# Kernel tuning notes

Measured on AMD Instinct MI355X. Metric: run time of the kernel, lower is better.

The kernel has to match this reference:

```python
import jax, jax.numpy as jnp
import numpy as np

B, C, K, F = 16, 64, 128, 6
HORIZON_S = 3.0  # conflict_horizon_s default
EPS = 1e-06


def setup_inputs() -> dict:
    rng = np.random.default_rng(0)
    # base adjacency: sparse random directed graph, zero diagonal
    A = (rng.random((B, K, K)) < 0.05).astype(np.float32)
    A[:, np.arange(K), np.arange(K)] = 0.0
    # candidates: exactly one unordered-pair edit (state in {0:none,1:i->j,2:j->i})
    cand = np.repeat(A[:, None], C, axis=1).copy()
    i = rng.integers(0, K - 1, (B, C))
    j = i + 1 + (rng.integers(0, K - 1, (B, C)) % (K - 1 - i))
    state = rng.integers(0, 3, (B, C))
    bidx = np.arange(B)[:, None] * np.ones((1, C), dtype=np.int64)
    cidx = np.ones((B, 1), dtype=np.int64) * np.arange(C)[None, :]
    cand[bidx, cidx, i, j] = (state == 1).astype(np.float32)
    cand[bidx, cidx, j, i] = (state == 2).astype(np.float32)
    cand[:, 0] = A  # candidate 0 is NOOP (keep A_t)
    # agent features: (x, y, yaw, vx, vy, pad)
    feat = rng.normal(size=(B, K, F)).astype(np.float32)
    feat[..., 0:2] *= 20.0  # spread positions over ~40m
    mask = (rng.random((B, K)) > 0.1).astype(np.float32)
    return {
        "A_t": jnp.asarray(A),
        "candidate_A": jnp.asarray(cand),
        "agent_feat": jnp.asarray(feat),
        "agent_mask": jnp.asarray(mask),
    }


def _edit_tokens(A_t, candidate_A):
    # vectorized version of EBSTM.extract_edit_tokens
    Bn, Cn, Kn, _ = candidate_A.shape
    base = A_t > 0.5                      # [B,K,K]
    cb = candidate_A > 0.5                # [B,C,K,K]
    diff = cb != base[:, None]            # [B,C,K,K]
    upper = jnp.triu(jnp.ones((Kn, Kn), dtype=bool), k=1)
    pairdiff = (diff | jnp.swapaxes(diff, -1, -2)) & upper
    flat = pairdiff.reshape(Bn, Cn, Kn * Kn)
    changed = flat.any(-1)                # [B,C]
    idx = jnp.argmax(flat, axis=-1)       # first changed pair in row-major (i,j) order
    i = idx // Kn
    j = idx % Kn
    barange = jnp.arange(Bn)[:, None]
    carange = jnp.arange(Cn)[None, :]
    b_ij = base[barange, i, j]
    b_ji = base[barange, j, i]
    c_ij = cb[barange, carange, i, j]
    c_ji = cb[barange, carange, j, i]
    prev = jnp.where(b_ij & ~b_ji, 1, jnp.where(b_ji & ~b_ij, 2, 0))
    nxt = jnp.where(c_ij & ~c_ji, 1, jnp.where(c_ji & ~c_ij, 2, 0))
    tokens = jnp.stack([i, j, prev, nxt], axis=-1).astype(jnp.int32)
    return tokens * changed[..., None].astype(jnp.int32)


def _relation_state3(cb):
    # cb: bool [B,C,K,K]
    at = jnp.swapaxes(cb, -1, -2)
    return ((cb & ~at).astype(jnp.int32) * 1
            + (~cb & at).astype(jnp.int32) * 2
            + (cb & at).astype(jnp.int32) * 3)


def _batched_acyclic(cb, agent_mask):
    # vectorized Kahn zero-indegree peel, matching EBSTM._is_acyclic semantics:
    #  - indegree counts edges from ALL sources (valid or not)
    #  - only valid nodes are ever removed
    #  - special case: <=1 valid node is acyclic
    Bn, Cn, Kn, _ = cb.shape
    valid = (agent_mask > 0.5)[:, None, :]           # [B,1,K]
    Ai = cb.astype(jnp.int32)                        # [B,C,K,K]
    indeg = Ai.sum(axis=-2) * valid.astype(jnp.int32)  # [B,C,K]
    removed = jnp.zeros((Bn, Cn, Kn), dtype=bool)

    def body(t, carry):
        indeg, removed = carry
        rem = valid & (~removed) & (indeg == 0)
        dec = jnp.einsum('bci,bcij->bcj', rem.astype(jnp.int32), Ai)
        return indeg - dec, removed | rem

    indeg, removed = jax.lax.fori_loop(0, Kn, body, (indeg, removed))
    vcount = valid.astype(jnp.int32).sum(-1)          # [B,1]
    return (removed.astype(jnp.int32).sum(-1) == vcount) | (vcount <= 1)


def _pair_dists(agent_feat):
    pos = agent_feat[..., 0:2]
    vel = agent_feat[..., 3:5]
    # _pair_distance: d[b,i,j] = |pos_i - pos_j|
    d = jnp.linalg.norm(pos[:, :, None] - pos[:, None, :], axis=-1)
    # _pair_closest_approach_distance: r[b,i,j] = pos_j - pos_i
    r = pos[:, None, :] - pos[:, :, None]
    v = vel[:, None, :] - vel[:, :, None]
    vv = (v * v).sum(-1)
    rv = (r * v).sum(-1)
    t_star = jnp.clip(-rv / (vv + EPS), 0.0, HORIZON_S)
    dmin = jnp.linalg.norm(r + v * t_star[..., None], axis=-1)
    eye = jnp.eye(dmin.shape[-1], dtype=bool)[None]
    dmin = jnp.where(eye, jnp.inf, dmin)
    return jnp.stack([d, dmin], axis=0)  # [2,B,K,K]


def reference(A_t, candidate_A, agent_feat, agent_mask):
    cb = candidate_A > 0.5
    tokens = _edit_tokens(A_t, candidate_A)          # [B,C,4] int32
    rel = _relation_state3(cb)                       # [B,C,K,K] int32
    acyclic = _batched_acyclic(cb, agent_mask)       # [B,C] bool
    dists = _pair_dists(agent_feat)                  # [2,B,K,K] float32
    return tokens, rel, acyclic, dists
```

## Files before the change

### kernel.cpp

```cpp
#include <hip/hip_runtime.h>
#include <cstdint>
#include <math.h>

#define KN 128
#define BATCH 16
#define CAND 64

typedef float vfloat4 __attribute__((ext_vector_type(4)));

static constexpr size_t TOK_OFF = 0;
static constexpr size_t REL_OFF = (size_t)BATCH * CAND * 4;
static constexpr size_t ACY_OFF = REL_OFF + (size_t)BATCH * CAND * KN * KN;
static constexpr size_t DST_OFF = ACY_OFF + (size_t)BATCH * CAND;

#define DIAG_BIG 1.0e30f

__global__ __launch_bounds__(256) void fused_kernel(const float* __restrict__ A_t,
                                                    const float* __restrict__ cand,
                                                    const float* __restrict__ feat,
                                                    const float* __restrict__ mask,
                                                    float* __restrict__ out) {
    __shared__ uint32_t adj[KN][5];
    __shared__ uint32_t adjW[4][KN];
    __shared__ uint32_t baseB[KN][4];
    __shared__ int      indegP[2][KN];
    __shared__ int      indeg[KN];
    __shared__ uint32_t validW[4];
    __shared__ uint32_t remW[4];
    __shared__ uint32_t removedW[4];
    __shared__ int      minIdx;

    const int t    = threadIdx.x;
    const int lane = t & 63;
    const int wave = t >> 6;
    const int bc   = blockIdx.x;
    const int b    = bc >> 6;

    const float* cptr = cand + (size_t)bc * (KN * KN);
    const float* aptr = A_t + (size_t)b * (KN * KN);

    if (t == 0) minIdx = 0x7fffffff;
    if (t < 4)  removedW[t] = 0;

    if (wave < 2) {
        float mv = mask[b * KN + wave * 64 + lane];
        unsigned long long m = __ballot(mv > 0.5f);
        if (lane == 0) {
            validW[wave * 2]     = (uint32_t)m;
            validW[wave * 2 + 1] = (uint32_t)(m >> 32);
        }
    }

    for (int m = 0; m < 16; ++m) {
        int rowPair = m * 4 + wave;
        int r   = rowPair * 2 + (lane >> 5);
        int sub = lane & 31;
        const float4 v = ((const float4*)(aptr + (size_t)r * KN))[sub];
        uint32_t nib = (v.x > 0.5f ? 1u : 0u) | (v.y > 0.5f ? 2u : 0u) |
                       (v.z > 0.5f ? 4u : 0u) | (v.w > 0.5f ? 8u : 0u);
        uint32_t word = nib << (4 * (sub & 7));
        word |= __shfl_xor(word, 1);
        word |= __shfl_xor(word, 2);
        word |= __shfl_xor(word, 4);
        if ((lane & 7) == 0) baseB[r][sub >> 3] = word;
    }

    for (int m = 0; m < 16; ++m) {
        int rowPair = m * 4 + wave;
        int r   = rowPair * 2 + (lane >> 5);
        int sub = lane & 31;
        const float4 v = ((const float4*)(cptr + (size_t)r * KN))[sub];
        uint32_t nib = (v.x > 0.5f ? 1u : 0u) | (v.y > 0.5f ? 2u : 0u) |
                       (v.z > 0.5f ? 4u : 0u) | (v.w > 0.5f ? 8u : 0u);
        uint32_t word = nib << (4 * (sub & 7));
        word |= __shfl_xor(word, 1);
        word |= __shfl_xor(word, 2);
        word |= __shfl_xor(word, 4);
        if ((lane & 7) == 0) adj[r][sub >> 3] = word;
    }

    {
        int bi = 2 * bc + (t >> 7);
        int b2 = bi >> 7, i = bi & 127, j = t & 127;
        const float* fi = feat + (size_t)bi * 6;
        const float* fj = feat + (size_t)(b2 * KN + j) * 6;
        float pix = fi[0], piy = fi[1], vix = fi[3], viy = fi[4];
        float pjx = fj[0], pjy = fj[1], vjx = fj[3], vjy = fj[4];
        float dx = pix - pjx, dy = piy - pjy;
        float d = sqrtf(dx * dx + dy * dy);
        float rx = pjx - pix, ry = pjy - piy;
        float vx = vjx - vix, vy = vjy - viy;
        float vv = vx * vx + vy * vy;
        float rv = rx * vx + ry * vy;
        float ts = fminf(fmaxf(-rv / (vv + 1e-6f), 0.0f), 3.0f);
        float mx = rx + vx * ts, my = ry + vy * ts;
        float dmin = (i == j) ? DIAG_BIG : sqrtf(mx * mx + my * my);
        float* o = out + DST_OFF;
        __builtin_nontemporal_store(d,    o + (size_t)(b2 * KN + i) * KN + j);
        __builtin_nontemporal_store(dmin, o + (size_t)((BATCH + b2) * KN + i) * KN + j);
    }
    __syncthreads();

    for (int w = t; w < 512; w += 256) {
        int iw = w >> 7, j = w & 127;
        adjW[iw][j] = adj[j][iw];
    }

    {
        int j = t & 127, half = t >> 7;
        uint32_t jw = j >> 5, jb = j & 31;
        int s = 0;
        int i0 = half * 64;
        for (int i = i0; i < i0 + 64; ++i) s += (adj[i][jw] >> jb) & 1u;
        indegP[half][j] = s;
    }

    for (int idx = t; idx < 512; idx += 256) {
        int i = idx >> 2, k = idx & 3;
        uint32_t diff = adj[i][k] ^ baseB[i][k];
        if (diff) {
            int base = k * 32;
            uint32_t up, low;
            if (i < base)            { up = diff; low = 0u; }
            else if (i >= base + 31) { up = 0u; low = (i > base + 31) ? diff : (diff & 0x7fffffffu); }
            else {
                int s = i - base;
                up  = diff & (0xffffffffu << (s + 1));
                low = diff & ((1u << s) - 1u);
            }
            int c1 = 0x7fffffff, c2 = 0x7fffffff;
            if (up)  c1 = (i << 7) | (base + __builtin_ctz(up));
            if (low) { int cc = base + __builtin_ctz(low); c2 = (cc << 7) | i; }
            int cm = min(c1, c2);
            if (cm != 0x7fffffff) atomicMin(&minIdx, cm);
        }
    }
    __syncthreads();

    if (t < KN) {
        uint32_t jw = t >> 5, jb = t & 31;
        bool valid = (validW[jw] >> jb) & 1u;
        indeg[t] = valid ? (indegP[0][t] + indegP[1][t]) : 0;
    }

    if (t == 0) {
        float* tok = out + TOK_OFF + (size_t)bc * 4;
        int mi = minIdx;
        if (mi != 0x7fffffff) {
            int i = mi >> 7, j = mi & 127;
            uint32_t b_ij = (baseB[i][j >> 5] >> (j & 31)) & 1u;
            uint32_t b_ji = (baseB[j][i >> 5] >> (i & 31)) & 1u;
            uint32_t c_ij = (adj[i][j >> 5] >> (j & 31)) & 1u;
            uint32_t c_ji = (adj[j][i >> 5] >> (i & 31)) & 1u;
            int prev = (b_ij && !b_ji) ? 1 : ((b_ji && !b_ij) ? 2 : 0);
            int nxt  = (c_ij && !c_ji) ? 1 : ((c_ji && !c_ij) ? 2 : 0);
            tok[0] = (float)i; tok[1] = (float)j; tok[2] = (float)prev; tok[3] = (float)nxt;
        } else {
            tok[0] = 0.f; tok[1] = 0.f; tok[2] = 0.f; tok[3] = 0.f;
        }
    }

    {
        float* relp = out + REL_OFF + (size_t)bc * (KN * KN);
        for (int m = 0; m < 16; ++m) {
            int q  = t + 256 * m;
            int i  = q >> 5;
            int j0 = (q & 31) * 4;
            uint32_t wij = adj[i][j0 >> 5];
            int sh = j0 & 31;
            uint32_t iw = i >> 5, ib = i & 31;
            const uint4 wt = *(const uint4*)&adjW[iw][j0];
            vfloat4 o;
            o.x = (float)(((wij >> (sh + 0)) & 1u) + 2u * ((wt.x >> ib) & 1u));
            o.y = (float)(((wij >> (sh + 1)) & 1u) + 2u * ((wt.y >> ib) & 1u));
            o.z = (float)(((wij >> (sh + 2)) & 1u) + 2u * ((wt.z >> ib) & 1u));
            o.w = (float)(((wij >> (sh + 3)) & 1u) + 2u * ((wt.w >> ib) & 1u));
            __builtin_nontemporal_store(o, ((vfloat4*)relp) + q);
        }
    }
    __syncthreads();

    for (int it = 0; it < KN; ++it) {
        bool rem = false;
        if (t < KN) {
            uint32_t jw = t >> 5, jb = t & 31;
            bool valid   = (validW[jw] >> jb) & 1u;
            bool removed = (removedW[jw] >> jb) & 1u;
            rem = valid && !removed && (indeg[t] == 0);
        }
        unsigned long long m = __ballot(rem);
        if (wave < 2 && lane == 0) {
            remW[wave * 2]     = (uint32_t)m;
            remW[wave * 2 + 1] = (uint32_t)(m >> 32);
        }
        __syncthreads();
        uint32_t r0 = remW[0], r1 = remW[1], r2 = remW[2], r3 = remW[3];
        if ((r0 | r1 | r2 | r3) == 0u) break;
        if (t < 4) removedW[t] |= remW[t];
        if (t < KN) {
            uint32_t jw = t >> 5, jb = t & 31;
            int dec = 0;
            uint32_t rw[4] = {r0, r1, r2, r3};
            for (int w = 0; w < 4; ++w) {
                uint32_t mm = rw[w];
                while (mm) {
                    int i = w * 32 + __builtin_ctz(mm);
                    mm &= mm - 1;
                    dec += (adj[i][jw] >> jb) & 1u;
                }
            }
            indeg[t] -= dec;
        }
        __syncthreads();
    }
    __syncthreads();

    if (t == 0) {
        int rc = __popc(removedW[0]) + __popc(removedW[1]) + __popc(removedW[2]) + __popc(removedW[3]);
        int vc = __popc(validW[0]) + __popc(validW[1]) + __popc(validW[2]) + __popc(validW[3]);
        out[ACY_OFF + bc] = ((rc == vc) || (vc <= 1)) ? 1.0f : 0.0f;
    }
}

extern "C" void kernel_launch(void* const* d_in, const int* in_sizes, int n_in,
                              void* d_out, int out_size, void* d_ws, size_t ws_size,
                              hipStream_t stream) {
    const float* A_t  = (const float*)d_in[0];
    const float* cand = (const float*)d_in[1];
    const float* feat = (const float*)d_in[2];
    const float* mask = (const float*)d_in[3];
    float* out = (float*)d_out;

    fused_kernel<<<BATCH * CAND, 256, 0, stream>>>(A_t, cand, feat, mask, out);
}
```

Baseline: 137.1 us.

## Precompute base adjacency bitmasks in a pre-kernel and prefetch candidate rows into registers

Measured after the change: 121.1 us. 11.6% less time.

```diff
diff --git a/kernel.cpp b/kernel.cpp
--- a/kernel.cpp
+++ b/kernel.cpp
@@ -15,11 +15,26 @@
 
 #define DIAG_BIG 1.0e30f
 
-__global__ __launch_bounds__(256) void fused_kernel(const float* __restrict__ A_t,
-                                                    const float* __restrict__ cand,
-                                                    const float* __restrict__ feat,
-                                                    const float* __restrict__ mask,
-                                                    float* __restrict__ out) {
+__global__ __launch_bounds__(256) void base_bits_kernel(const float* __restrict__ A_t,
+                                                        uint32_t* __restrict__ bits) {
+    int tid  = blockIdx.x * 256 + threadIdx.x;
+    int wave = tid >> 6;
+    int lane = tid & 63;
+    int half = wave & 1;
+    int row  = wave >> 1;
+    float v = A_t[(size_t)row * KN + half * 64 + lane];
+    unsigned long long m = __ballot(v > 0.5f);
+    if (lane == 0) {
+        bits[row * 4 + half * 2]     = (uint32_t)m;
+        bits[row * 4 + half * 2 + 1] = (uint32_t)(m >> 32);
+    }
+}
+
+__global__ __launch_bounds__(256) void main_kernel(const float* __restrict__ cand,
+                                                   const float* __restrict__ feat,
+                                                   const float* __restrict__ mask,
+                                                   const uint32_t* __restrict__ baseBits,
+                                                   float* __restrict__ out) {
     __shared__ uint32_t adj[KN][5];
     __shared__ uint32_t adjW[4][KN];
     __shared__ uint32_t baseB[KN][4];
@@ -37,10 +52,21 @@
     const int b    = bc >> 6;
 
     const float* cptr = cand + (size_t)bc * (KN * KN);
-    const float* aptr = A_t + (size_t)b * (KN * KN);
+
+    float4 c[16];
+    const int sub = lane & 31;
+    #pragma unroll
+    for (int m = 0; m < 16; ++m) {
+        int r = (m * 4 + wave) * 2 + (lane >> 5);
+        c[m] = ((const float4*)(cptr + (size_t)r * KN))[sub];
+    }
 
     if (t == 0) minIdx = 0x7fffffff;
     if (t < 4)  removedW[t] = 0;
+
+    for (int w = t; w < 512; w += 256) {
+        baseB[w >> 2][w & 3] = baseBits[b * 512 + w];
+    }
 
     if (wave < 2) {
         float mv = mask[b * KN + wave * 64 + lane];
@@ -49,34 +75,6 @@
             validW[wave * 2]     = (uint32_t)m;
             validW[wave * 2 + 1] = (uint32_t)(m >> 32);
         }
-    }
-
-    for (int m = 0; m < 16; ++m) {
-        int rowPair = m * 4 + wave;
-        int r   = rowPair * 2 + (lane >> 5);
-        int sub = lane & 31;
-        const float4 v = ((const float4*)(aptr + (size_t)r * KN))[sub];
-        uint32_t nib = (v.x > 0.5f ? 1u : 0u) | (v.y > 0.5f ? 2u : 0u) |
-                       (v.z > 0.5f ? 4u : 0u) | (v.w > 0.5f ? 8u : 0u);
-        uint32_t word = nib << (4 * (sub & 7));
-        word |= __shfl_xor(word, 1);
-        word |= __shfl_xor(word, 2);
-        word |= __shfl_xor(word, 4);
-        if ((lane & 7) == 0) baseB[r][sub >> 3] = word;
-    }
-
-    for (int m = 0; m < 16; ++m) {
-        int rowPair = m * 4 + wave;
-        int r   = rowPair * 2 + (lane >> 5);
-        int sub = lane & 31;
-        const float4 v = ((const float4*)(cptr + (size_t)r * KN))[sub];
-        uint32_t nib = (v.x > 0.5f ? 1u : 0u) | (v.y > 0.5f ? 2u : 0u) |
-                       (v.z > 0.5f ? 4u : 0u) | (v.w > 0.5f ? 8u : 0u);
-        uint32_t word = nib << (4 * (sub & 7));
-        word |= __shfl_xor(word, 1);
-        word |= __shfl_xor(word, 2);
-        word |= __shfl_xor(word, 4);
-        if ((lane & 7) == 0) adj[r][sub >> 3] = word;
     }
 
     {
@@ -99,6 +97,19 @@
         __builtin_nontemporal_store(d,    o + (size_t)(b2 * KN + i) * KN + j);
         __builtin_nontemporal_store(dmin, o + (size_t)((BATCH + b2) * KN + i) * KN + j);
     }
+
+    #pragma unroll
+    for (int m = 0; m < 16; ++m) {
+        int r = (m * 4 + wave) * 2 + (lane >> 5);
+        const float4 v = c[m];
+        uint32_t nib = (v.x > 0.5f ? 1u : 0u) | (v.y > 0.5f ? 2u : 0u) |
+                       (v.z > 0.5f ? 4u : 0u) | (v.w > 0.5f ? 8u : 0u);
+        uint32_t word = nib << (4 * (sub & 7));
+        word |= __shfl_xor(word, 1);
+        word |= __shfl_xor(word, 2);
+        word |= __shfl_xor(word, 4);
+        if ((lane & 7) == 0) adj[r][sub >> 3] = word;
+    }
     __syncthreads();
 
     for (int w = t; w < 512; w += 256) {
@@ -162,6 +173,7 @@
 
     {
         float* relp = out + REL_OFF + (size_t)bc * (KN * KN);
+        #pragma unroll 4
         for (int m = 0; m < 16; ++m) {
             int q  = t + 256 * m;
             int i  = q >> 5;
@@ -230,6 +242,8 @@
     const float* feat = (const float*)d_in[2];
     const float* mask = (const float*)d_in[3];
     float* out = (float*)d_out;
-
-    fused_kernel<<<BATCH * CAND, 256, 0, stream>>>(A_t, cand, feat, mask, out);
+    uint32_t* bits = (uint32_t*)d_ws;
+
+    base_bits_kernel<<<1024, 256, 0, stream>>>(A_t, bits);
+    main_kernel<<<BATCH * CAND, 256, 0, stream>>>(cand, feat, mask, bits, out);
 }
```

## Split fused kernel into specialized block roles for rel, acyclic, and distances

Applied to the files above, without the earlier changes.

After: 136.3 us. Within noise of the previous version (-0.6%).

```diff
diff --git a/kernel.cpp b/kernel.cpp
--- a/kernel.cpp
+++ b/kernel.cpp
@@ -15,13 +15,12 @@
 
 #define DIAG_BIG 1.0e30f
 
-__global__ __launch_bounds__(256) void fused_kernel(const float* __restrict__ A_t,
-                                                    const float* __restrict__ cand,
-                                                    const float* __restrict__ feat,
-                                                    const float* __restrict__ mask,
-                                                    float* __restrict__ out) {
+__global__ __launch_bounds__(256) void mega_kernel(const float* __restrict__ A_t,
+                                                   const float* __restrict__ cand,
+                                                   const float* __restrict__ feat,
+                                                   const float* __restrict__ mask,
+                                                   float* __restrict__ out) {
     __shared__ uint32_t adj[KN][5];
-    __shared__ uint32_t adjW[4][KN];
     __shared__ uint32_t baseB[KN][4];
     __shared__ int      indegP[2][KN];
     __shared__ int      indeg[KN];
@@ -29,58 +28,230 @@
     __shared__ uint32_t remW[4];
     __shared__ uint32_t removedW[4];
     __shared__ int      minIdx;
+    __shared__ uint32_t adjH[64][5];
+    __shared__ uint32_t adjTW[2][KN];
 
     const int t    = threadIdx.x;
     const int lane = t & 63;
     const int wave = t >> 6;
-    const int bc   = blockIdx.x;
-    const int b    = bc >> 6;
-
-    const float* cptr = cand + (size_t)bc * (KN * KN);
-    const float* aptr = A_t + (size_t)b * (KN * KN);
-
-    if (t == 0) minIdx = 0x7fffffff;
-    if (t < 4)  removedW[t] = 0;
-
-    if (wave < 2) {
-        float mv = mask[b * KN + wave * 64 + lane];
-        unsigned long long m = __ballot(mv > 0.5f);
-        if (lane == 0) {
-            validW[wave * 2]     = (uint32_t)m;
-            validW[wave * 2 + 1] = (uint32_t)(m >> 32);
-        }
-    }
-
-    for (int m = 0; m < 16; ++m) {
-        int rowPair = m * 4 + wave;
-        int r   = rowPair * 2 + (lane >> 5);
-        int sub = lane & 31;
-        const float4 v = ((const float4*)(aptr + (size_t)r * KN))[sub];
-        uint32_t nib = (v.x > 0.5f ? 1u : 0u) | (v.y > 0.5f ? 2u : 0u) |
-                       (v.z > 0.5f ? 4u : 0u) | (v.w > 0.5f ? 8u : 0u);
-        uint32_t word = nib << (4 * (sub & 7));
-        word |= __shfl_xor(word, 1);
-        word |= __shfl_xor(word, 2);
-        word |= __shfl_xor(word, 4);
-        if ((lane & 7) == 0) baseB[r][sub >> 3] = word;
-    }
-
-    for (int m = 0; m < 16; ++m) {
-        int rowPair = m * 4 + wave;
-        int r   = rowPair * 2 + (lane >> 5);
-        int sub = lane & 31;
-        const float4 v = ((const float4*)(cptr + (size_t)r * KN))[sub];
-        uint32_t nib = (v.x > 0.5f ? 1u : 0u) | (v.y > 0.5f ? 2u : 0u) |
-                       (v.z > 0.5f ? 4u : 0u) | (v.w > 0.5f ? 8u : 0u);
-        uint32_t word = nib << (4 * (sub & 7));
-        word |= __shfl_xor(word, 1);
-        word |= __shfl_xor(word, 2);
-        word |= __shfl_xor(word, 4);
-        if ((lane & 7) == 0) adj[r][sub >> 3] = word;
-    }
-
-    {
-        int bi = 2 * bc + (t >> 7);
+    const int blk  = blockIdx.x;
+
+    if (blk < 2048) {
+        const int bc = blk >> 1;
+        const int h  = blk & 1;
+        const float* cptr = cand + (size_t)bc * (KN * KN);
+
+        float4 cr[8], cc[8];
+        const int sub   = lane & 31;
+        const int sub16 = lane & 15;
+        #pragma unroll
+        for (int m = 0; m < 8; ++m) {
+            int r = (m * 4 + wave) * 2 + (lane >> 5);
+            cr[m] = ((const float4*)(cptr + (size_t)(h * 64 + r) * KN))[sub];
+        }
+        #pragma unroll
+        for (int m = 0; m < 8; ++m) {
+            int j = m * 16 + wave * 4 + (lane >> 4);
+            cc[m] = ((const float4*)(cptr + (size_t)j * KN + h * 64))[sub16];
+        }
+
+        #pragma unroll
+        for (int m = 0; m < 8; ++m) {
+            int r = (m * 4 + wave) * 2 + (lane >> 5);
+            float4 v = cr[m];
+            uint32_t nib = (v.x > 0.5f ? 1u : 0u) | (v.y > 0.5f ? 2u : 0u) |
+                           (v.z > 0.5f ? 4u : 0u) | (v.w > 0.5f ? 8u : 0u);
+            uint32_t word = nib << (4 * (sub & 7));
+            word |= __shfl_xor(word, 1);
+            word |= __shfl_xor(word, 2);
+            word |= __shfl_xor(word, 4);
+            if ((lane & 7) == 0) adjH[r][sub >> 3] = word;
+        }
+        #pragma unroll
+        for (int m = 0; m < 8; ++m) {
+            int j = m * 16 + wave * 4 + (lane >> 4);
+            float4 v = cc[m];
+            uint32_t nib = (v.x > 0.5f ? 1u : 0u) | (v.y > 0.5f ? 2u : 0u) |
+                           (v.z > 0.5f ? 4u : 0u) | (v.w > 0.5f ? 8u : 0u);
+            uint32_t word = nib << (4 * (sub16 & 7));
+            word |= __shfl_xor(word, 1);
+            word |= __shfl_xor(word, 2);
+            word |= __shfl_xor(word, 4);
+            if ((sub16 & 7) == 0) adjTW[sub16 >> 3][j] = word;
+        }
+        __syncthreads();
+
+        float* relp = out + REL_OFF + (size_t)bc * (KN * KN);
+        #pragma unroll
+        for (int m = 0; m < 8; ++m) {
+            int q  = t + 256 * m;
+            int il = q >> 5;
+            int j0 = (q & 31) * 4;
+            uint32_t wij = adjH[il][j0 >> 5];
+            int sh = j0 & 31;
+            uint32_t ib = il & 31;
+            const uint4 wt = *(const uint4*)&adjTW[il >> 5][j0];
+            vfloat4 o;
+            o.x = (float)(((wij >> (sh + 0)) & 1u) + 2u * ((wt.x >> ib) & 1u));
+            o.y = (float)(((wij >> (sh + 1)) & 1u) + 2u * ((wt.y >> ib) & 1u));
+            o.z = (float)(((wij >> (sh + 2)) & 1u) + 2u * ((wt.z >> ib) & 1u));
+            o.w = (float)(((wij >> (sh + 3)) & 1u) + 2u * ((wt.w >> ib) & 1u));
+            __builtin_nontemporal_store(o, ((vfloat4*)relp) + (size_t)h * 2048 + q);
+        }
+    } else if (blk < 3072) {
+        const int bc = blk - 2048;
+        const int b  = bc >> 6;
+        const float* cptr = cand + (size_t)bc * (KN * KN);
+        const float* aptr = A_t + (size_t)b * (KN * KN);
+        const int sub = lane & 31;
+
+        float4 c[16];
+        #pragma unroll
+        for (int m = 0; m < 16; ++m) {
+            int r = (m * 4 + wave) * 2 + (lane >> 5);
+            c[m] = ((const float4*)(cptr + (size_t)r * KN))[sub];
+        }
+
+        if (t == 0) minIdx = 0x7fffffff;
+        if (t < 4)  removedW[t] = 0;
+
+        if (wave < 2) {
+            float mv = mask[b * KN + wave * 64 + lane];
+            unsigned long long m = __ballot(mv > 0.5f);
+            if (lane == 0) {
+                validW[wave * 2]     = (uint32_t)m;
+                validW[wave * 2 + 1] = (uint32_t)(m >> 32);
+            }
+        }
+
+        #pragma unroll
+        for (int m = 0; m < 16; ++m) {
+            int r = (m * 4 + wave) * 2 + (lane >> 5);
+            float4 v = c[m];
+            uint32_t nib = (v.x > 0.5f ? 1u : 0u) | (v.y > 0.5f ? 2u : 0u) |
+                           (v.z > 0.5f ? 4u : 0u) | (v.w > 0.5f ? 8u : 0u);
+            uint32_t word = nib << (4 * (sub & 7));
+            word |= __shfl_xor(word, 1);
+            word |= __shfl_xor(word, 2);
+            word |= __shfl_xor(word, 4);
+            if ((lane & 7) == 0) adj[r][sub >> 3] = word;
+        }
+        #pragma unroll
+        for (int m = 0; m < 16; ++m) {
+            int r = (m * 4 + wave) * 2 + (lane >> 5);
+            c[m] = ((const float4*)(aptr + (size_t)r * KN))[sub];
+        }
+        #pragma unroll
+        for (int m = 0; m < 16; ++m) {
+            int r = (m * 4 + wave) * 2 + (lane >> 5);
+            float4 v = c[m];
+            uint32_t nib = (v.x > 0.5f ? 1u : 0u) | (v.y > 0.5f ? 2u : 0u) |
+                           (v.z > 0.5f ? 4u : 0u) | (v.w > 0.5f ? 8u : 0u);
+            uint32_t word = nib << (4 * (sub & 7));
+            word |= __shfl_xor(word, 1);
+            word |= __shfl_xor(word, 2);
+            word |= __shfl_xor(word, 4);
+            if ((lane & 7) == 0) baseB[r][sub >> 3] = word;
+        }
+        __syncthreads();
+
+        {
+            int j = t & 127, half = t >> 7;
+            uint32_t jw = j >> 5, jb = j & 31;
+            int s = 0;
+            int i0 = half * 64;
+            for (int i = i0; i < i0 + 64; ++i) s += (adj[i][jw] >> jb) & 1u;
+            indegP[half][j] = s;
+        }
+
+        for (int idx = t; idx < 512; idx += 256) {
+            int i = idx >> 2, k = idx & 3;
+            uint32_t diff = adj[i][k] ^ baseB[i][k];
+            if (diff) {
+                int base = k * 32;
+                uint32_t up, low;
+                if (i < base)            { up = diff; low = 0u; }
+                else if (i >= base + 31) { up = 0u; low = (i > base + 31) ? diff : (diff & 0x7fffffffu); }
+                else {
+                    int s = i - base;
+                    up  = diff & (0xffffffffu << (s + 1));
+                    low = diff & ((1u << s) - 1u);
+                }
+                int c1 = 0x7fffffff, c2 = 0x7fffffff;
+                if (up)  c1 = (i << 7) | (base + __builtin_ctz(up));
+                if (low) { int cc = base + __builtin_ctz(low); c2 = (cc << 7) | i; }
+                int cm = min(c1, c2);
+                if (cm != 0x7fffffff) atomicMin(&minIdx, cm);
+            }
+        }
+        __syncthreads();
+
+        if (t < KN) {
+            uint32_t jw = t >> 5, jb = t & 31;
+            bool valid = (validW[jw] >> jb) & 1u;
+            indeg[t] = valid ? (indegP[0][t] + indegP[1][t]) : 0;
+        }
+
+        if (t == 0) {
+            float* tok = out + TOK_OFF + (size_t)bc * 4;
+            int mi = minIdx;
+            if (mi != 0x7fffffff) {
+                int i = mi >> 7, j = mi & 127;
+                uint32_t b_ij = (baseB[i][j >> 5] >> (j & 31)) & 1u;
+                uint32_t b_ji = (baseB[j][i >> 5] >> (i & 31)) & 1u;
+                uint32_t c_ij = (adj[i][j >> 5] >> (j & 31)) & 1u;
+                uint32_t c_ji = (adj[j][i >> 5] >> (i & 31)) & 1u;
+                int prev = (b_ij && !b_ji) ? 1 : ((b_ji && !b_ij) ? 2 : 0);
+                int nxt  = (c_ij && !c_ji) ? 1 : ((c_ji && !c_ij) ? 2 : 0);
+                tok[0] = (float)i; tok[1] = (float)j; tok[2] = (float)prev; tok[3] = (float)nxt;
+            } else {
+                tok[0] = 0.f; tok[1] = 0.f; tok[2] = 0.f; tok[3] = 0.f;
+            }
+        }
+        __syncthreads();
+
+        for (int it = 0; it < KN; ++it) {
+            bool rem = false;
+            if (t < KN) {
+                uint32_t jw = t >> 5, jb = t & 31;
+                bool valid   = (validW[jw] >> jb) & 1u;
+                bool removed = (removedW[jw] >> jb) & 1u;
+                rem = valid && !removed && (indeg[t] == 0);
+            }
+            unsigned long long m = __ballot(rem);
+            if (wave < 2 && lane == 0) {
+                remW[wave * 2]     = (uint32_t)m;
+                remW[wave * 2 + 1] = (uint32_t)(m >> 32);
+            }
+            __syncthreads();
+            uint32_t r0 = remW[0], r1 = remW[1], r2 = remW[2], r3 = remW[3];
+            if ((r0 | r1 | r2 | r3) == 0u) break;
+            if (t < 4) removedW[t] |= remW[t];
+            if (t < KN) {
+                uint32_t jw = t >> 5, jb = t & 31;
+                int dec = 0;
+                uint32_t rw[4] = {r0, r1, r2, r3};
+                for (int w = 0; w < 4; ++w) {
+                    uint32_t mm = rw[w];
+                    while (mm) {
+                        int i = w * 32 + __builtin_ctz(mm);
+                        mm &= mm - 1;
+                        dec += (adj[i][jw] >> jb) & 1u;
+                    }
+                }
+                indeg[t] -= dec;
+            }
+            __syncthreads();
+        }
+        __syncthreads();
+
+        if (t == 0) {
+            int rc = __popc(removedW[0]) + __popc(removedW[1]) + __popc(removedW[2]) + __popc(removedW[3]);
+            int vc = __popc(validW[0]) + __popc(validW[1]) + __popc(validW[2]) + __popc(validW[3]);
+            out[ACY_OFF + bc] = ((rc == vc) || (vc <= 1)) ? 1.0f : 0.0f;
+        }
+    } else {
+        int bi = 2 * (blk - 3072) + (t >> 7);
         int b2 = bi >> 7, i = bi & 127, j = t & 127;
         const float* fi = feat + (size_t)bi * 6;
         const float* fj = feat + (size_t)(b2 * KN + j) * 6;
@@ -99,127 +270,6 @@
         __builtin_nontemporal_store(d,    o + (size_t)(b2 * KN + i) * KN + j);
         __builtin_nontemporal_store(dmin, o + (size_t)((BATCH + b2) * KN + i) * KN + j);
     }
-    __syncthreads();
-
-    for (int w = t; w < 512; w += 256) {
-        int iw = w >> 7, j = w & 127;
-        adjW[iw][j] = adj[j][iw];
-    }
-
-    {
-        int j = t & 127, half = t >> 7;
-        uint32_t jw = j >> 5, jb = j & 31;
-        int s = 0;
-        int i0 = half * 64;
-        for (int i = i0; i < i0 + 64; ++i) s += (adj[i][jw] >> jb) & 1u;
-        indegP[half][j] = s;
-    }
-
-    for (int idx = t; idx < 512; idx += 256) {
-        int i = idx >> 2, k = idx & 3;
-        uint32_t diff = adj[i][k] ^ baseB[i][k];
-        if (diff) {
-            int base = k * 32;
-            uint32_t up, low;
-            if (i < base)            { up = diff; low = 0u; }
-            else if (i >= base + 31) { up = 0u; low = (i > base + 31) ? diff : (diff & 0x7fffffffu); }
-            else {
-                int s = i - base;
-                up  = diff & (0xffffffffu << (s + 1));
-                low = diff & ((1u << s) - 1u);
-            }
-            int c1 = 0x7fffffff, c2 = 0x7fffffff;
-            if (up)  c1 = (i << 7) | (base + __builtin_ctz(up));
-            if (low) { int cc = base + __builtin_ctz(low); c2 = (cc << 7) | i; }
-            int cm = min(c1, c2);
-            if (cm != 0x7fffffff) atomicMin(&minIdx, cm);
-        }
-    }
-    __syncthreads();
-
-    if (t < KN) {
-        uint32_t jw = t >> 5, jb = t & 31;
-        bool valid = (validW[jw] >> jb) & 1u;
-        indeg[t] = valid ? (indegP[0][t] + indegP[1][t]) : 0;
-    }
-
-    if (t == 0) {
-        float* tok = out + TOK_OFF + (size_t)bc * 4;
-        int mi = minIdx;
-        if (mi != 0x7fffffff) {
-            int i = mi >> 7, j = mi & 127;
-            uint32_t b_ij = (baseB[i][j >> 5] >> (j & 31)) & 1u;
-            uint32_t b_ji = (baseB[j][i >> 5] >> (i & 31)) & 1u;
-            uint32_t c_ij = (adj[i][j >> 5] >> (j & 31)) & 1u;
-            uint32_t c_ji = (adj[j][i >> 5] >> (i & 31)) & 1u;
-            int prev = (b_ij && !b_ji) ? 1 : ((b_ji && !b_ij) ? 2 : 0);
-            int nxt  = (c_ij && !c_ji) ? 1 : ((c_ji && !c_ij) ? 2 : 0);
-            tok[0] = (float)i; tok[1] = (float)j; tok[2] = (float)prev; tok[3] = (float)nxt;
-        } else {
-            tok[0] = 0.f; tok[1] = 0.f; tok[2] = 0.f; tok[3] = 0.f;
-        }
-    }
-
-    {
-        float* relp = out + REL_OFF + (size_t)bc * (KN * KN);
-        for (int m = 0; m < 16; ++m) {
-            int q  = t + 256 * m;
-            int i  = q >> 5;
-            int j0 = (q & 31) * 4;
-            uint32_t wij = adj[i][j0 >> 5];
-            int sh = j0 & 31;
-            uint32_t iw = i >> 5, ib = i & 31;
-            const uint4 wt = *(const uint4*)&adjW[iw][j0];
-            vfloat4 o;
-            o.x = (float)(((wij >> (sh + 0)) & 1u) + 2u * ((wt.x >> ib) & 1u));
-            o.y = (float)(((wij >> (sh + 1)) & 1u) + 2u * ((wt.y >> ib) & 1u));
-            o.z = (float)(((wij >> (sh + 2)) & 1u) + 2u * ((wt.z >> ib) & 1u));
-            o.w = (float)(((wij >> (sh + 3)) & 1u) + 2u * ((wt.w >> ib) & 1u));
-            __builtin_nontemporal_store(o, ((vfloat4*)relp) + q);
-        }
-    }
-    __syncthreads();
-
-    for (int it = 0; it < KN; ++it) {
-        bool rem = false;
-        if (t < KN) {
-            uint32_t jw = t >> 5, jb = t & 31;
-            bool valid   = (validW[jw] >> jb) & 1u;
-            bool removed = (removedW[jw] >> jb) & 1u;
-            rem = valid && !removed && (indeg[t] == 0);
-        }
-        unsigned long long m = __ballot(rem);
-        if (wave < 2 && lane == 0) {
-            remW[wave * 2]     = (uint32_t)m;
-            remW[wave * 2 + 1] = (uint32_t)(m >> 32);
-        }
-        __syncthreads();
-        uint32_t r0 = remW[0], r1 = remW[1], r2 = remW[2], r3 = remW[3];
-        if ((r0 | r1 | r2 | r3) == 0u) break;
-        if (t < 4) removedW[t] |= remW[t];
-        if (t < KN) {
-            uint32_t jw = t >> 5, jb = t & 31;
-            int dec = 0;
-            uint32_t rw[4] = {r0, r1, r2, r3};
-            for (int w = 0; w < 4; ++w) {
-                uint32_t mm = rw[w];
-                while (mm) {
-                    int i = w * 32 + __builtin_ctz(mm);
-                    mm &= mm - 1;
-                    dec += (adj[i][jw] >> jb) & 1u;
-                }
-            }
-            indeg[t] -= dec;
-        }
-        __syncthreads();
-    }
-    __syncthreads();
-
-    if (t == 0) {
-        int rc = __popc(removedW[0]) + __popc(removedW[1]) + __popc(removedW[2]) + __popc(removedW[3]);
-        int vc = __popc(validW[0]) + __popc(validW[1]) + __popc(validW[2]) + __popc(validW[3]);
-        out[ACY_OFF + bc] = ((rc == vc) || (vc <= 1)) ? 1.0f : 0.0f;
-    }
 }
 
 extern "C" void kernel_launch(void* const* d_in, const int* in_sizes, int n_in,
@@ -231,5 +281,5 @@
     const float* mask = (const float*)d_in[3];
     float* out = (float*)d_out;
 
-    fused_kernel<<<BATCH * CAND, 256, 0, stream>>>(A_t, cand, feat, mask, out);
+    mega_kernel<<<4096, 256, 0, stream>>>(A_t, cand, feat, mask, out);
 }
```
